# Kernel tuning notes

Measured on AMD Instinct MI355X. Metric: run time of the kernel, lower is better.

Reference implementation:

```python
import jax, jax.numpy as jnp
import numpy as np

MARGIN = 0.1

def setup_inputs() -> dict:
    key = jax.random.key(0)
    k1, k2, k3 = jax.random.split(key, 3)
    B, P, N, D = 512, 4, 64, 1024
    return {
        "query_emb": jax.random.normal(k1, (B, D), dtype=jnp.float32),
        "pos_emb": jax.random.normal(k2, (B, P, D), dtype=jnp.float32),
        "neg_emb": jax.random.normal(k3, (B, N, D), dtype=jnp.float32),
    }

def reference(query_emb, pos_emb, neg_emb):
    # pos_scores: [B, P], neg_scores: [B, N]
    pos_scores = jnp.einsum("bd,bpd->bp", query_emb, pos_emb)
    neg_scores = jnp.einsum("bd,bnd->bn", query_emb, neg_emb)
    # Original: sum_{i,j} mean_b relu(margin - pos[:,i] + neg[:,j]) / (P*N)
    # == mean over (b, i, j) of relu(margin - pos[b,i] + neg[b,j])
    pairwise = jax.nn.relu(MARGIN - pos_scores[:, :, None] + neg_scores[:, None, :])
    return jnp.mean(pairwise)
```

## Files before the change

kernel.cpp:

```cpp
#include <hip/hip_runtime.h>
#include <hip/hip_bf16.h>

#define MARGIN 0.1f
#define B 512
#define P 4
#define N 64
#define D 1024
#define NV (P + N)

__global__ __launch_bounds__(1024) void scores_kernel(
    const float* __restrict__ q,
    const float* __restrict__ pos,
    const float* __restrict__ neg,
    float* __restrict__ partial)
{
    const int b    = blockIdx.x;
    const int tid  = threadIdx.x;
    const int lane = tid & 63;
    const int wave = tid >> 6;

    const float4* q4 = (const float4*)(q + (size_t)b * D);
    float4 qv[4];
#pragma unroll
    for (int i = 0; i < 4; ++i) qv[i] = q4[i * 64 + lane];

    __shared__ float scores[NV];

    for (int v = wave; v < NV; v += 16) {
        const float* vec = (v < P)
            ? (pos + ((size_t)b * P + v) * D)
            : (neg + ((size_t)b * N + (v - P)) * D);
        const float4* v4 = (const float4*)vec;
        float acc = 0.0f;
#pragma unroll
        for (int i = 0; i < 4; ++i) {
            float4 x = v4[i * 64 + lane];
            acc += qv[i].x * x.x + qv[i].y * x.y + qv[i].z * x.z + qv[i].w * x.w;
        }
#pragma unroll
        for (int off = 32; off > 0; off >>= 1)
            acc += __shfl_down(acc, off, 64);
        if (lane == 0) scores[v] = acc;
    }
    __syncthreads();

    __shared__ float wsum[4];
    if (wave < 4) {
        float ps  = scores[wave];
        float ns  = scores[P + lane];
        float val = fmaxf(MARGIN - ps + ns, 0.0f);
#pragma unroll
        for (int off = 32; off > 0; off >>= 1)
            val += __shfl_down(val, off, 64);
        if (lane == 0) wsum[wave] = val;
    }
    __syncthreads();
    if (tid == 0)
        partial[b] = wsum[0] + wsum[1] + wsum[2] + wsum[3];
}

__global__ __launch_bounds__(64) void finalize_kernel(
    const float* __restrict__ partial, float* __restrict__ out)
{
    const int lane = threadIdx.x;
    float v = 0.0f;
#pragma unroll
    for (int k = 0; k < 8; ++k)
        v += partial[lane + 64 * k];
#pragma unroll
    for (int off = 32; off > 0; off >>= 1)
        v += __shfl_down(v, off, 64);
    if (lane == 0)
        out[0] = v / (float)(B * P * N);
}

extern "C" void kernel_launch(void* const* d_in, const int* in_sizes, int n_in,
                              void* d_out, int out_size, void* d_ws, size_t ws_size,
                              hipStream_t stream) {
    const float* q   = (const float*)d_in[0];
    const float* pos = (const float*)d_in[1];
    const float* neg = (const float*)d_in[2];
    float* out       = (float*)d_out;
    float* partial   = (float*)d_ws;

    scores_kernel<<<B, 1024, 0, stream>>>(q, pos, neg, partial);
    finalize_kernel<<<1, 64, 0, stream>>>(partial, out);
}
```

Baseline: 27.93 us.

## Fuse score and finalize kernels into one cooperative launch with grid sync

Merges the per-batch scoring kernel and the single-block finalize kernel into one cooperative kernel launched with 256 blocks, each handling two batch rows in sequence. Partials are written with agent-scope atomic stores, then a grid-wide sync lets block 0 do the final reduction. This removes the second kernel launch and its dependency gap. In exchange it halves the grid so each block processes rows serially, and it pays for a grid barrier and cooperative launch overhead.

```diff
diff --git a/kernel.cpp b/kernel.cpp
--- a/kernel.cpp
+++ b/kernel.cpp
@@ -1,5 +1,7 @@
 #include <hip/hip_runtime.h>
-#include <hip/hip_bf16.h>
+#include <hip/hip_cooperative_groups.h>
+
+namespace cg = cooperative_groups;
 
 #define MARGIN 0.1f
 #define B 512
@@ -7,71 +9,81 @@
 #define N 64
 #define D 1024
 #define NV (P + N)
+#define GRID 256
+#define REP (B / GRID)
 
-__global__ __launch_bounds__(1024) void scores_kernel(
+__global__ __launch_bounds__(1024) void loss_kernel(
     const float* __restrict__ q,
     const float* __restrict__ pos,
     const float* __restrict__ neg,
-    float* __restrict__ partial)
+    float* __restrict__ partial,
+    float* __restrict__ out)
 {
-    const int b    = blockIdx.x;
     const int tid  = threadIdx.x;
     const int lane = tid & 63;
     const int wave = tid >> 6;
 
-    const float4* q4 = (const float4*)(q + (size_t)b * D);
-    float4 qv[4];
+    __shared__ float scores[NV];
+    __shared__ float wsum[4];
+
+    for (int rep = 0; rep < REP; ++rep) {
+        const int b = (int)blockIdx.x + rep * GRID;
+
+        const float4* q4 = (const float4*)(q + (size_t)b * D);
+        float4 qv[4];
 #pragma unroll
-    for (int i = 0; i < 4; ++i) qv[i] = q4[i * 64 + lane];
+        for (int i = 0; i < 4; ++i) qv[i] = q4[i * 64 + lane];
 
-    __shared__ float scores[NV];
+        for (int v = wave; v < NV; v += 16) {
+            const float* vec = (v < P)
+                ? (pos + ((size_t)b * P + v) * D)
+                : (neg + ((size_t)b * N + (v - P)) * D);
+            const float4* v4 = (const float4*)vec;
+            float acc = 0.0f;
+#pragma unroll
+            for (int i = 0; i < 4; ++i) {
+                float4 x = v4[i * 64 + lane];
+                acc += qv[i].x * x.x + qv[i].y * x.y + qv[i].z * x.z + qv[i].w * x.w;
+            }
+#pragma unroll
+            for (int off = 32; off > 0; off >>= 1)
+                acc += __shfl_down(acc, off, 64);
+            if (lane == 0) scores[v] = acc;
+        }
+        __syncthreads();
 
-    for (int v = wave; v < NV; v += 16) {
-        const float* vec = (v < P)
-            ? (pos + ((size_t)b * P + v) * D)
-            : (neg + ((size_t)b * N + (v - P)) * D);
-        const float4* v4 = (const float4*)vec;
-        float acc = 0.0f;
+        if (wave < 4) {
+            float ps  = scores[wave];
+            float ns  = scores[P + lane];
+            float val = fmaxf(MARGIN - ps + ns, 0.0f);
 #pragma unroll
-        for (int i = 0; i < 4; ++i) {
-            float4 x = v4[i * 64 + lane];
-            acc += qv[i].x * x.x + qv[i].y * x.y + qv[i].z * x.z + qv[i].w * x.w;
+            for (int off = 32; off > 0; off >>= 1)
+                val += __shfl_down(val, off, 64);
+            if (lane == 0) wsum[wave] = val;
         }
+        __syncthreads();
+
+        if (tid == 0) {
+            float s = wsum[0] + wsum[1] + wsum[2] + wsum[3];
+            __hip_atomic_store(&partial[b], s, __ATOMIC_RELAXED,
+                               __HIP_MEMORY_SCOPE_AGENT);
+        }
+    }
+
+    cg::this_grid().sync();
+
+    if (blockIdx.x == 0 && wave == 0) {
+        float v = 0.0f;
+#pragma unroll
+        for (int k = 0; k < 8; ++k)
+            v += __hip_atomic_load(&partial[lane + 64 * k], __ATOMIC_RELAXED,
+                                   __HIP_MEMORY_SCOPE_AGENT);
 #pragma unroll
         for (int off = 32; off > 0; off >>= 1)
-            acc += __shfl_down(acc, off, 64);
-        if (lane == 0) scores[v] = acc;
+            v += __shfl_down(v, off, 64);
+        if (lane == 0)
+            out[0] = v / (float)(B * P * N);
     }
-    __syncthreads();
-
-    __shared__ float wsum[4];
-    if (wave < 4) {
-        float ps  = scores[wave];
-        float ns  = scores[P + lane];
-        float val = fmaxf(MARGIN - ps + ns, 0.0f);
-#pragma unroll
-        for (int off = 32; off > 0; off >>= 1)
-            val += __shfl_down(val, off, 64);
-        if (lane == 0) wsum[wave] = val;
-    }
-    __syncthreads();
-    if (tid == 0)
-        partial[b] = wsum[0] + wsum[1] + wsum[2] + wsum[3];
-}
-
-__global__ __launch_bounds__(64) void finalize_kernel(
-    const float* __restrict__ partial, float* __restrict__ out)
-{
-    const int lane = threadIdx.x;
-    float v = 0.0f;
-#pragma unroll
-    for (int k = 0; k < 8; ++k)
-        v += partial[lane + 64 * k];
-#pragma unroll
-    for (int off = 32; off > 0; off >>= 1)
-        v += __shfl_down(v, off, 64);
-    if (lane == 0)
-        out[0] = v / (float)(B * P * N);
 }
 
 extern "C" void kernel_launch(void* const* d_in, const int* in_sizes, int n_in,
@@ -83,6 +95,8 @@
     float* out       = (float*)d_out;
     float* partial   = (float*)d_ws;
 
-    scores_kernel<<<B, 1024, 0, stream>>>(q, pos, neg, partial);
-    finalize_kernel<<<1, 64, 0, stream>>>(partial, out);
+    void* args[] = { (void*)&q, (void*)&pos, (void*)&neg,
+                     (void*)&partial, (void*)&out };
+    hipLaunchCooperativeKernel((const void*)loss_kernel,
+                               dim3(GRID), dim3(1024), args, 0, stream);
 }
```

Measured after the change: 69.89 us. 150% more time.
